# Kernel optimization log

Measured on AMD Instinct MI355X. Metric: run time of the kernel, lower is better.

## Reference

```python
import jax, jax.numpy as jnp
import numpy as np

IN_DIM = 64
OUT_DIM = 16  # SPD matrix side
HIDDEN = [128, 128]
CHOL_DIM = OUT_DIM + OUT_DIM * (OUT_DIM - 1) // 2  # 136
BATCH = 65536
LEAKY_SLOPE = 0.01  # torch.nn.LeakyReLU default


def _uniform(key, shape, in_feat):
    b = 1.0 / in_feat
    return jax.random.uniform(key, shape, jnp.float32, -b, b)


def setup_inputs() -> dict:
    key = jax.random.key(0)
    ks = jax.random.split(key, 7)
    x = jax.random.normal(ks[0], (BATCH, IN_DIM), jnp.float32)
    # layer sizes: 64 -> 128 -> 128 -> 136, init uniform(-1/in_feat, 1/in_feat)
    W1 = _uniform(ks[1], (IN_DIM, HIDDEN[0]), IN_DIM)
    b1 = _uniform(ks[2], (HIDDEN[0],), IN_DIM)
    W2 = _uniform(ks[3], (HIDDEN[0], HIDDEN[1]), HIDDEN[0])
    b2 = _uniform(ks[4], (HIDDEN[1],), HIDDEN[0])
    W3 = _uniform(ks[5], (HIDDEN[1], CHOL_DIM), HIDDEN[1])
    b3 = _uniform(ks[6], (CHOL_DIM,), HIDDEN[1])
    return {"x": x, "W1": W1, "b1": b1, "W2": W2, "b2": b2, "W3": W3, "b3": b3}


def reference(x, W1, b1, W2, b2, W3, b3):
    # MLP with LeakyReLU between layers, then Tanh on final output
    h = jax.nn.leaky_relu(x @ W1 + b1, LEAKY_SLOPE)
    h = jax.nn.leaky_relu(h @ W2 + b2, LEAKY_SLOPE)
    ldata = jnp.tanh(h @ W3 + b3)  # [B, 136]

    # fill_tril: scatter the 136 values into the lower triangle (row-major)
    rows, cols = jnp.tril_indices(OUT_DIM)
    L = jnp.zeros((x.shape[0], OUT_DIM, OUT_DIM), x.dtype).at[:, rows, cols].set(ldata)
    Q = L + jnp.swapaxes(L, -1, -2)  # symmetric [B, 16, 16]

    # symmetric eigendecomposition (ascending eigenvalues, like torch.symeig)
    w, V = jnp.linalg.eigh(Q)
    # sqrt(softmax(exp(w)**2)) ; exp(w)**2 == exp(2w)
    ev = jnp.sqrt(jax.nn.softmax(jnp.exp(2.0 * w), axis=-1))  # [B, 16]
    # faithful to source: uses inverse (== V^T in exact math since V orthogonal)
    Vinv = jnp.linalg.inv(V)
    # V @ diag(ev) @ V^{-1}
    return jnp.einsum('bij,bj,bjk->bik', V, ev, Vinv)
```

## Files before the change

kernel.cpp:

```cpp
#include <hip/hip_runtime.h>
#include <math.h>

typedef _Float16 f16;
typedef _Float16 half4_t __attribute__((ext_vector_type(4)));
typedef _Float16 half8_t __attribute__((ext_vector_type(8)));
typedef float floatx4 __attribute__((ext_vector_type(4)));

__global__ __launch_bounds__(256) void prep_weights(
    const float* __restrict__ W1, const float* __restrict__ W2,
    const float* __restrict__ W3, f16* __restrict__ wt) {
  int t = blockIdx.x * 256 + threadIdx.x;
  if (t < 8192) {
    int c = t >> 6, k = t & 63;
    wt[t] = (f16)W1[k * 128 + c];
  } else if (t < 24576) {
    int u = t - 8192;
    int c = u >> 7, k = u & 127;
    wt[t] = (f16)W2[k * 128 + c];
  } else if (t < 43008) {
    int u = t - 24576;
    int c = u >> 7, k = u & 127;
    wt[t] = (f16)((c < 136) ? W3[k * 136 + c] : 0.0f);
  }
}

__device__ __forceinline__ float fast_tanh(float v) {
  float e = __builtin_amdgcn_exp2f(v * 2.885390081777926814f);
  return 1.0f - 2.0f * __builtin_amdgcn_rcpf(e + 1.0f);
}

template <int CTRL>
__device__ __forceinline__ float dpp_add(float v) {
  int t = __builtin_amdgcn_update_dpp(0, __builtin_bit_cast(int, v), CTRL,
                                      0xf, 0xf, true);
  return v + __builtin_bit_cast(float, t);
}
__device__ __forceinline__ float wsum(float v) {
  v = dpp_add<0x111>(v);
  v = dpp_add<0x112>(v);
  v = dpp_add<0x114>(v);
  v = dpp_add<0x118>(v);
  v = dpp_add<0x142>(v);
  v = dpp_add<0x143>(v);
  return __builtin_bit_cast(
      float, __builtin_amdgcn_readlane(__builtin_bit_cast(int, v), 63));
}

__device__ __forceinline__ half4_t to_h(floatx4 v) {
  auto p0 = __builtin_amdgcn_cvt_pkrtz(v[0], v[1]);
  auto p1 = __builtin_amdgcn_cvt_pkrtz(v[2], v[3]);
  half4_t h;
  h[0] = p0[0]; h[1] = p0[1]; h[2] = p1[0]; h[3] = p1[1];
  return h;
}

__device__ __forceinline__ floatx4 expm_c(floatx4 b, floatx4 I4, float& m) {
  float s2 = wsum(b[0] * b[0] + b[1] * b[1] + b[2] * b[2] + b[3] * b[3]);
  float td = wsum(I4[0] * b[0] + I4[1] * b[1] + I4[2] * b[2] + I4[3] * b[3]);
  m = td * 0.0625f;
  float fr2 = fmaxf(s2 - td * m, 1e-30f);
  int e2 = (int)(__builtin_bit_cast(unsigned, fr2) >> 23) - 127;
  int s = (e2 + 5) >> 1;
  s = s < 0 ? 0 : (s > 12 ? 12 : s);
  s = __builtin_amdgcn_readfirstlane(s);
  float sc = __builtin_bit_cast(float, (unsigned)(127 - s) << 23);
  b = (b - I4 * m) * sc;
  half4_t bh = to_h(b);
  floatx4 zero = {0.f, 0.f, 0.f, 0.f};
  floatx4 a2 = __builtin_amdgcn_mfma_f32_16x16x16f16(bh, bh, zero, 0, 0, 0);
  floatx4 t = I4 * 0.5f + b * (1.f / 6.f) + a2 * (1.f / 24.f);
  floatx4 p = __builtin_amdgcn_mfma_f32_16x16x16f16(to_h(a2), to_h(t), I4 + b,
                                                    0, 0, 0);
  for (int k = 0; k < s; ++k) {
    half4_t ph = to_h(p);
    p = __builtin_amdgcn_mfma_f32_16x16x16f16(ph, ph, zero, 0, 0, 0);
  }
  return p;
}

__global__ __launch_bounds__(64) void fused_kernel(
    const float* __restrict__ x, const float* __restrict__ b1,
    const float* __restrict__ b2v, const float* __restrict__ b3,
    const f16* __restrict__ wt, float* __restrict__ out) {
  __shared__ f16 hb[16][136];
  const int lane = threadIdx.x & 63;
  const int cl = lane & 15;
  const int q = lane >> 4;
  const int r0 = blockIdx.x * 16;

  const f16* w1t = wt;
  const f16* w2t = wt + 8192;
  const f16* w3t = wt + 24576;

  half8_t a0, a1;
  {
    const float* xr = x + (size_t)(r0 + cl) * 64 + q * 8;
    floatx4 v0 = *(const floatx4*)(xr);
    floatx4 v1 = *(const floatx4*)(xr + 4);
    floatx4 v2 = *(const floatx4*)(xr + 32);
    floatx4 v3 = *(const floatx4*)(xr + 36);
#pragma unroll
    for (int i = 0; i < 4; ++i) {
      a0[i] = (f16)v0[i]; a0[i + 4] = (f16)v1[i];
      a1[i] = (f16)v2[i]; a1[i + 4] = (f16)v3[i];
    }
  }
#pragma unroll
  for (int c8 = 0; c8 < 8; ++c8) {
    int c = c8 * 16 + cl;
    half8_t w0 = *(const half8_t*)(w1t + c * 64 + q * 8);
    half8_t w1v = *(const half8_t*)(w1t + c * 64 + 32 + q * 8);
    floatx4 acc = {0.f, 0.f, 0.f, 0.f};
    acc = __builtin_amdgcn_mfma_f32_16x16x32_f16(a0, w0, acc, 0, 0, 0);
    acc = __builtin_amdgcn_mfma_f32_16x16x32_f16(a1, w1v, acc, 0, 0, 0);
    float bias = b1[c];
#pragma unroll
    for (int i = 0; i < 4; ++i) {
      float v = acc[i] + bias;
      v = v > 0.f ? v : 0.01f * v;
      hb[q * 4 + i][c] = (f16)v;
    }
  }

  half8_t ha[4];
#pragma unroll
  for (int ks = 0; ks < 4; ++ks)
    ha[ks] = *(const half8_t*)(&hb[cl][ks * 32 + q * 8]);
#pragma unroll
  for (int c8 = 0; c8 < 8; ++c8) {
    int c = c8 * 16 + cl;
    floatx4 acc = {0.f, 0.f, 0.f, 0.f};
#pragma unroll
    for (int ks = 0; ks < 4; ++ks) {
      half8_t wv = *(const half8_t*)(w2t + c * 128 + ks * 32 + q * 8);
      acc = __builtin_amdgcn_mfma_f32_16x16x32_f16(ha[ks], wv, acc, 0, 0, 0);
    }
    float bias = b2v[c];
#pragma unroll
    for (int i = 0; i < 4; ++i) {
      float v = acc[i] + bias;
      v = v > 0.f ? v : 0.01f * v;
      hb[q * 4 + i][c] = (f16)v;
    }
  }

#pragma unroll
  for (int ks = 0; ks < 4; ++ks)
    ha[ks] = *(const half8_t*)(&hb[cl][ks * 32 + q * 8]);
#pragma unroll
  for (int c8 = 0; c8 < 9; ++c8) {
    int c = c8 * 16 + cl;
    floatx4 acc = {0.f, 0.f, 0.f, 0.f};
#pragma unroll
    for (int ks = 0; ks < 4; ++ks) {
      half8_t wv = *(const half8_t*)(w3t + c * 128 + ks * 32 + q * 8);
      acc = __builtin_amdgcn_mfma_f32_16x16x32_f16(ha[ks], wv, acc, 0, 0, 0);
    }
    if (c < 136) {
      float bias = b3[c];
#pragma unroll
      for (int i = 0; i < 4; ++i)
        hb[q * 4 + i][c] = (f16)fast_tanh(acc[i] + bias);
    }
  }

  unsigned triOff[4];
  floatx4 I4, c4v;
#pragma unroll
  for (int i = 0; i < 4; ++i) {
    int k = q * 4 + i;
    int hi = cl > k ? cl : k;
    int lo = cl + k - hi;
    triOff[i] = (unsigned)(hi * (hi + 1) / 2 + lo) * 2u;
    bool d = (cl == k);
    I4[i] = d ? 1.f : 0.f;
    c4v[i] = d ? 4.f : 2.f;
  }

  for (int mt = 0; mt < 16; ++mt) {
    const char* base = (const char*)&hb[mt][0];
    floatx4 b;
#pragma unroll
    for (int i = 0; i < 4; ++i)
      b[i] = c4v[i] * (float)*(const f16*)(base + triOff[i]);

    float m1;
    floatx4 p = expm_c(b, I4, m1);
    float fac = __builtin_amdgcn_exp2f(m1 * 1.4426950408889634f - 1.0f);
    float m2;
    p = expm_c(p * fac, I4, m2);

    float n2 = wsum(p[0] * p[0] + p[1] * p[1] + p[2] * p[2] + p[3] * p[3]);
    float inv = __builtin_amdgcn_rsqf(n2);
    floatx4 o = p * inv;
    *(floatx4*)(out + (size_t)(r0 + mt) * 256 + cl * 16 + q * 4) = o;
  }
}

extern "C" void kernel_launch(void* const* d_in, const int* in_sizes, int n_in,
                              void* d_out, int out_size, void* d_ws,
                              size_t ws_size, hipStream_t stream) {
  const float* x = (const float*)d_in[0];
  const float* W1 = (const float*)d_in[1];
  const float* b1 = (const float*)d_in[2];
  const float* W2 = (const float*)d_in[3];
  const float* b2 = (const float*)d_in[4];
  const float* W3 = (const float*)d_in[5];
  const float* b3 = (const float*)d_in[6];
  float* out = (float*)d_out;
  f16* wt = (f16*)d_ws;

  prep_weights<<<168, 256, 0, stream>>>(W1, W2, W3, wt);
  fused_kernel<<<4096, 64, 0, stream>>>(x, b1, b2, b3, wt, out);
}
```

Measured before the change: 145.3 us.

## Split fused kernel into MLP kernel and per-matrix expm kernel

Replaces the single fused kernel, where one wave ran the MLP for 16 rows and then serially computed 16 matrix exponentials, with two kernels. An MLP kernel uses 4 waves per block and writes the tanh outputs as fp16 to workspace. An expm kernel then assigns one wave per matrix, giving 65536 independent waves. This removes the serial 16-iteration expm loop per wave and raises parallelism, at the cost of an extra launch and a global round-trip of the fp16 ldata buffer (about 17 MB).

```diff
diff --git a/kernel.cpp b/kernel.cpp
--- a/kernel.cpp
+++ b/kernel.cpp
@@ -5,6 +5,8 @@
 typedef _Float16 half4_t __attribute__((ext_vector_type(4)));
 typedef _Float16 half8_t __attribute__((ext_vector_type(8)));
 typedef float floatx4 __attribute__((ext_vector_type(4)));
+
+#define LDATA_OFF_BYTES 86016
 
 __global__ __launch_bounds__(256) void prep_weights(
     const float* __restrict__ W1, const float* __restrict__ W2,
@@ -27,6 +29,97 @@
 __device__ __forceinline__ float fast_tanh(float v) {
   float e = __builtin_amdgcn_exp2f(v * 2.885390081777926814f);
   return 1.0f - 2.0f * __builtin_amdgcn_rcpf(e + 1.0f);
+}
+
+__global__ __launch_bounds__(256) void mlp_kernel(
+    const float* __restrict__ x, const float* __restrict__ b1,
+    const float* __restrict__ b2v, const float* __restrict__ b3,
+    const f16* __restrict__ wt, f16* __restrict__ ldata) {
+  __shared__ f16 hb[2][4][16][136];
+  const int tid = threadIdx.x;
+  const int wave = tid >> 6;
+  const int lane = tid & 63;
+  const int cl = lane & 15;
+  const int q = lane >> 4;
+  const int r0 = blockIdx.x * 64 + wave * 16;
+
+  const f16* w1t = wt;
+  const f16* w2t = wt + 8192;
+  const f16* w3t = wt + 24576;
+
+  half8_t a0, a1;
+  {
+    const float* xr = x + (size_t)(r0 + cl) * 64 + q * 8;
+    floatx4 v0 = *(const floatx4*)(xr);
+    floatx4 v1 = *(const floatx4*)(xr + 4);
+    floatx4 v2 = *(const floatx4*)(xr + 32);
+    floatx4 v3 = *(const floatx4*)(xr + 36);
+#pragma unroll
+    for (int i = 0; i < 4; ++i) {
+      a0[i] = (f16)v0[i]; a0[i + 4] = (f16)v1[i];
+      a1[i] = (f16)v2[i]; a1[i + 4] = (f16)v3[i];
+    }
+  }
+#pragma unroll
+  for (int c8 = 0; c8 < 8; ++c8) {
+    int c = c8 * 16 + cl;
+    half8_t w0 = *(const half8_t*)(w1t + c * 64 + q * 8);
+    half8_t w1v = *(const half8_t*)(w1t + c * 64 + 32 + q * 8);
+    floatx4 acc = {0.f, 0.f, 0.f, 0.f};
+    acc = __builtin_amdgcn_mfma_f32_16x16x32_f16(a0, w0, acc, 0, 0, 0);
+    acc = __builtin_amdgcn_mfma_f32_16x16x32_f16(a1, w1v, acc, 0, 0, 0);
+    float bias = b1[c];
+#pragma unroll
+    for (int i = 0; i < 4; ++i) {
+      float v = acc[i] + bias;
+      v = v > 0.f ? v : 0.01f * v;
+      hb[0][wave][q * 4 + i][c] = (f16)v;
+    }
+  }
+  __syncthreads();
+
+  half8_t ha[4];
+#pragma unroll
+  for (int ks = 0; ks < 4; ++ks)
+    ha[ks] = *(const half8_t*)(&hb[0][wave][cl][ks * 32 + q * 8]);
+#pragma unroll
+  for (int c8 = 0; c8 < 8; ++c8) {
+    int c = c8 * 16 + cl;
+    floatx4 acc = {0.f, 0.f, 0.f, 0.f};
+#pragma unroll
+    for (int ks = 0; ks < 4; ++ks) {
+      half8_t wv = *(const half8_t*)(w2t + c * 128 + ks * 32 + q * 8);
+      acc = __builtin_amdgcn_mfma_f32_16x16x32_f16(ha[ks], wv, acc, 0, 0, 0);
+    }
+    float bias = b2v[c];
+#pragma unroll
+    for (int i = 0; i < 4; ++i) {
+      float v = acc[i] + bias;
+      v = v > 0.f ? v : 0.01f * v;
+      hb[1][wave][q * 4 + i][c] = (f16)v;
+    }
+  }
+  __syncthreads();
+
+#pragma unroll
+  for (int ks = 0; ks < 4; ++ks)
+    ha[ks] = *(const half8_t*)(&hb[1][wave][cl][ks * 32 + q * 8]);
+#pragma unroll
+  for (int c8 = 0; c8 < 9; ++c8) {
+    int c = c8 * 16 + cl;
+    floatx4 acc = {0.f, 0.f, 0.f, 0.f};
+#pragma unroll
+    for (int ks = 0; ks < 4; ++ks) {
+      half8_t wv = *(const half8_t*)(w3t + c * 128 + ks * 32 + q * 8);
+      acc = __builtin_amdgcn_mfma_f32_16x16x32_f16(ha[ks], wv, acc, 0, 0, 0);
+    }
+    if (c < 136) {
+      float bias = b3[c];
+#pragma unroll
+      for (int i = 0; i < 4; ++i)
+        ldata[(size_t)(r0 + q * 4 + i) * 136 + c] = (f16)fast_tanh(acc[i] + bias);
+    }
+  }
 }
 
 template <int CTRL>
@@ -78,123 +171,35 @@
   return p;
 }
 
-__global__ __launch_bounds__(64) void fused_kernel(
-    const float* __restrict__ x, const float* __restrict__ b1,
-    const float* __restrict__ b2v, const float* __restrict__ b3,
-    const f16* __restrict__ wt, float* __restrict__ out) {
-  __shared__ f16 hb[16][136];
+__global__ __launch_bounds__(256) void expm_kernel(
+    const f16* __restrict__ ldata, float* __restrict__ out) {
   const int lane = threadIdx.x & 63;
-  const int cl = lane & 15;
-  const int q = lane >> 4;
-  const int r0 = blockIdx.x * 16;
-
-  const f16* w1t = wt;
-  const f16* w2t = wt + 8192;
-  const f16* w3t = wt + 24576;
-
-  half8_t a0, a1;
-  {
-    const float* xr = x + (size_t)(r0 + cl) * 64 + q * 8;
-    floatx4 v0 = *(const floatx4*)(xr);
-    floatx4 v1 = *(const floatx4*)(xr + 4);
-    floatx4 v2 = *(const floatx4*)(xr + 32);
-    floatx4 v3 = *(const floatx4*)(xr + 36);
-#pragma unroll
-    for (int i = 0; i < 4; ++i) {
-      a0[i] = (f16)v0[i]; a0[i + 4] = (f16)v1[i];
-      a1[i] = (f16)v2[i]; a1[i + 4] = (f16)v3[i];
-    }
-  }
-#pragma unroll
-  for (int c8 = 0; c8 < 8; ++c8) {
-    int c = c8 * 16 + cl;
-    half8_t w0 = *(const half8_t*)(w1t + c * 64 + q * 8);
-    half8_t w1v = *(const half8_t*)(w1t + c * 64 + 32 + q * 8);
-    floatx4 acc = {0.f, 0.f, 0.f, 0.f};
-    acc = __builtin_amdgcn_mfma_f32_16x16x32_f16(a0, w0, acc, 0, 0, 0);
-    acc = __builtin_amdgcn_mfma_f32_16x16x32_f16(a1, w1v, acc, 0, 0, 0);
-    float bias = b1[c];
-#pragma unroll
-    for (int i = 0; i < 4; ++i) {
-      float v = acc[i] + bias;
-      v = v > 0.f ? v : 0.01f * v;
-      hb[q * 4 + i][c] = (f16)v;
-    }
-  }
-
-  half8_t ha[4];
-#pragma unroll
-  for (int ks = 0; ks < 4; ++ks)
-    ha[ks] = *(const half8_t*)(&hb[cl][ks * 32 + q * 8]);
-#pragma unroll
-  for (int c8 = 0; c8 < 8; ++c8) {
-    int c = c8 * 16 + cl;
-    floatx4 acc = {0.f, 0.f, 0.f, 0.f};
-#pragma unroll
-    for (int ks = 0; ks < 4; ++ks) {
-      half8_t wv = *(const half8_t*)(w2t + c * 128 + ks * 32 + q * 8);
-      acc = __builtin_amdgcn_mfma_f32_16x16x32_f16(ha[ks], wv, acc, 0, 0, 0);
-    }
-    float bias = b2v[c];
-#pragma unroll
-    for (int i = 0; i < 4; ++i) {
-      float v = acc[i] + bias;
-      v = v > 0.f ? v : 0.01f * v;
-      hb[q * 4 + i][c] = (f16)v;
-    }
-  }
-
-#pragma unroll
-  for (int ks = 0; ks < 4; ++ks)
-    ha[ks] = *(const half8_t*)(&hb[cl][ks * 32 + q * 8]);
-#pragma unroll
-  for (int c8 = 0; c8 < 9; ++c8) {
-    int c = c8 * 16 + cl;
-    floatx4 acc = {0.f, 0.f, 0.f, 0.f};
-#pragma unroll
-    for (int ks = 0; ks < 4; ++ks) {
-      half8_t wv = *(const half8_t*)(w3t + c * 128 + ks * 32 + q * 8);
-      acc = __builtin_amdgcn_mfma_f32_16x16x32_f16(ha[ks], wv, acc, 0, 0, 0);
-    }
-    if (c < 136) {
-      float bias = b3[c];
-#pragma unroll
-      for (int i = 0; i < 4; ++i)
-        hb[q * 4 + i][c] = (f16)fast_tanh(acc[i] + bias);
-    }
-  }
-
-  unsigned triOff[4];
-  floatx4 I4, c4v;
+  const int mat = (int)((blockIdx.x * 256u + threadIdx.x) >> 6);
+  const int r = lane & 15, q = lane >> 4;
+  const f16* ld = ldata + (size_t)mat * 136;
+
+  floatx4 b, I4;
 #pragma unroll
   for (int i = 0; i < 4; ++i) {
     int k = q * 4 + i;
-    int hi = cl > k ? cl : k;
-    int lo = cl + k - hi;
-    triOff[i] = (unsigned)(hi * (hi + 1) / 2 + lo) * 2u;
-    bool d = (cl == k);
+    int hi = r > k ? r : k;
+    int lo = r + k - hi;
+    float v = (float)ld[hi * (hi + 1) / 2 + lo];
+    bool d = (r == k);
     I4[i] = d ? 1.f : 0.f;
-    c4v[i] = d ? 4.f : 2.f;
-  }
-
-  for (int mt = 0; mt < 16; ++mt) {
-    const char* base = (const char*)&hb[mt][0];
-    floatx4 b;
-#pragma unroll
-    for (int i = 0; i < 4; ++i)
-      b[i] = c4v[i] * (float)*(const f16*)(base + triOff[i]);
-
-    float m1;
-    floatx4 p = expm_c(b, I4, m1);
-    float fac = __builtin_amdgcn_exp2f(m1 * 1.4426950408889634f - 1.0f);
-    float m2;
-    p = expm_c(p * fac, I4, m2);
-
-    float n2 = wsum(p[0] * p[0] + p[1] * p[1] + p[2] * p[2] + p[3] * p[3]);
-    float inv = __builtin_amdgcn_rsqf(n2);
-    floatx4 o = p * inv;
-    *(floatx4*)(out + (size_t)(r0 + mt) * 256 + cl * 16 + q * 4) = o;
-  }
+    b[i] = d ? 4.f * v : 2.f * v;
+  }
+
+  float m1;
+  floatx4 p = expm_c(b, I4, m1);
+  float fac = __builtin_amdgcn_exp2f(m1 * 1.4426950408889634f - 1.0f);
+  float m2;
+  p = expm_c(p * fac, I4, m2);
+
+  float n2 = wsum(p[0] * p[0] + p[1] * p[1] + p[2] * p[2] + p[3] * p[3]);
+  float inv = __builtin_amdgcn_rsqf(n2);
+  floatx4 o = p * inv;
+  *(floatx4*)(out + (size_t)mat * 256 + r * 16 + q * 4) = o;
 }
 
 extern "C" void kernel_launch(void* const* d_in, const int* in_sizes, int n_in,
@@ -209,7 +214,9 @@
   const float* b3 = (const float*)d_in[6];
   float* out = (float*)d_out;
   f16* wt = (f16*)d_ws;
+  f16* ldata = (f16*)((char*)d_ws + LDATA_OFF_BYTES);
 
   prep_weights<<<168, 256, 0, stream>>>(W1, W2, W3, wt);
-  fused_kernel<<<4096, 64, 0, stream>>>(x, b1, b2, b3, wt, out);
-}
+  mlp_kernel<<<1024, 256, 0, stream>>>(x, b1, b2, b3, wt, ldata);
+  expm_kernel<<<16384, 256, 0, stream>>>(ldata, out);
+}
```

Measured after the change: 148.9 us. +2.4%, slower.
